# Kernel tuning notes

Hardware: AMD Instinct MI355X
Metric: run time of the kernel (lower is better)

The kernel has to match this reference:

```python
import math
import jax, jax.numpy as jnp
import numpy as np

B, Q, K = 1, 2048, 2048
CQ = CK = CV = 128
H, CH = 8, 32
HD = H * CH  # 256


def setup_inputs() -> dict:
    key = jax.random.key(0)
    ks = jax.random.split(key, 12)
    s = 0.02
    return {
        "q_x": jax.random.normal(ks[0], (B, Q, CQ), jnp.float32),
        "kv_x": jax.random.normal(ks[1], (B, K, CK), jnp.float32),
        "bias": jax.random.normal(ks[2], (B, 1, Q, K), jnp.float32),
        "distance": jax.random.uniform(ks[3], (B, Q, K, H), jnp.float32),
        "Wq": jax.random.normal(ks[4], (CQ, HD), jnp.float32) * s,
        "Wk": jax.random.normal(ks[5], (CK, HD), jnp.float32) * s,
        "Wv": jax.random.normal(ks[6], (CV, HD), jnp.float32) * s,
        "Wg": jax.random.normal(ks[7], (CQ, HD), jnp.float32) * s,
        "bg": jnp.zeros((HD,), jnp.float32),
        "Wo": jax.random.normal(ks[8], (HD, CQ), jnp.float32) * s,
        "bo": jnp.zeros((CQ,), jnp.float32),
    }


def reference(q_x, kv_x, bias, distance, Wq, Wk, Wv, Wg, bg, Wo, bo):
    # Projections -> [B, S, H, CH]
    q = (q_x @ Wq).reshape(B, Q, H, CH) / math.sqrt(CH)
    k = (kv_x @ Wk).reshape(B, K, H, CH)
    v = (kv_x @ Wv).reshape(B, K, H, CH)
    # Scores [B, H, Q, K]
    a = jnp.einsum("bqhc,bkhc->bhqk", q, k)
    a = a + bias
    # mha_permu=True: distance [B,Q,K,H] -> [B,H,Q,K]; rel_dis_pair_bias='add'
    a = a + jnp.transpose(distance, (0, 3, 1, 2))
    a = jax.nn.softmax(a, axis=-1)
    o = jnp.einsum("bhqk,bkhc->bqhc", a, v)  # [B, Q, H, CH]
    # Gating
    g = jax.nn.sigmoid(q_x @ Wg + bg).reshape(B, Q, H, CH)
    o = o * g
    o = o.reshape(B, Q, HD)
    return o @ Wo + bo
```

## Files before the change

kernel.cpp:

```cpp
#include <hip/hip_runtime.h>
#include <hip/hip_bf16.h>

#define Qn 2048
#define Kn 2048
#define Cin 128
#define Hn 8
#define CHn 32
#define HDn 256
#define NSPLIT 8
#define KP 68

typedef __attribute__((ext_vector_type(8))) short short8;
typedef __attribute__((ext_vector_type(4))) float f32x4;

static __device__ __forceinline__ unsigned short f2bf(float f) {
    unsigned int u = __float_as_uint(f);
    u += 0x7fffu + ((u >> 16) & 1u);
    return (unsigned short)(u >> 16);
}

__global__ __launch_bounds__(256) void proj_kernel(
    const float* __restrict__ qx, const float* __restrict__ kvx,
    const float* __restrict__ Wq, const float* __restrict__ Wk,
    const float* __restrict__ Wv, const float* __restrict__ Wg,
    const float* __restrict__ bg,
    unsigned short* __restrict__ qb, unsigned short* __restrict__ kb,
    unsigned short* __restrict__ vtb, float* __restrict__ gb)
{
    const int mat = blockIdx.y;
    const int r0 = blockIdx.x * 8;
    const int j = threadIdx.x;
    const float* A = (mat == 0 || mat == 3) ? qx : kvx;
    const float* W = (mat == 0) ? Wq : (mat == 1) ? Wk : (mat == 2) ? Wv : Wg;
    const float* Ar = A + r0 * Cin;
    float acc[8] = {0.f, 0.f, 0.f, 0.f, 0.f, 0.f, 0.f, 0.f};
    for (int c = 0; c < Cin; ++c) {
        const float w = W[c * HDn + j];
        #pragma unroll
        for (int i = 0; i < 8; ++i)
            acc[i] = fmaf(Ar[i * Cin + c], w, acc[i]);
    }
    if (mat == 0) {
        const float s = 0.17677669529663687f;
        #pragma unroll
        for (int i = 0; i < 8; ++i)
            qb[(r0 + i) * HDn + j] = f2bf(acc[i] * s);
    } else if (mat == 1) {
        #pragma unroll
        for (int i = 0; i < 8; ++i)
            kb[(r0 + i) * HDn + j] = f2bf(acc[i]);
    } else if (mat == 2) {
        unsigned short tmp[8];
        #pragma unroll
        for (int i = 0; i < 8; ++i) tmp[i] = f2bf(acc[i]);
        *(short8*)(vtb + (size_t)j * Kn + r0) = *(short8*)tmp;
    } else {
        const float b = bg[j];
        #pragma unroll
        for (int i = 0; i < 8; ++i)
            gb[(r0 + i) * HDn + j] = 1.f / (1.f + __expf(-(acc[i] + b)));
    }
}

__global__ __launch_bounds__(512, 5) void attn_kernel(
    const unsigned short* __restrict__ qb, const unsigned short* __restrict__ kb,
    const unsigned short* __restrict__ vtb,
    const float* __restrict__ bias, const float* __restrict__ dist,
    float* __restrict__ opart, float* __restrict__ lpart)
{
    __shared__ unsigned short ps[Hn][16][72];
    __shared__ _Float16 dbl[Hn * 16 * KP];

    const int bx = blockIdx.x;
    const int qt = bx >> 3;
    const int sp = bx & 7;
    const int q0 = qt * 16;
    const int k00 = sp * 256;
    const int t = threadIdx.x;
    const int h = t >> 6;
    const int l = t & 63;
    const int g = l >> 4;
    const int n = l & 15;

    const int sk = (t >> 1) & 63;
    const int shg = t & 1;
    const int sqb = t >> 7;

    const short8 qf = *(const short8*)(qb + (q0 + n) * HDn + h * CHn + g * 8);

    f32x4 o0 = {0.f, 0.f, 0.f, 0.f};
    f32x4 o1 = {0.f, 0.f, 0.f, 0.f};
    float lacc[4] = {0.f, 0.f, 0.f, 0.f};
    unsigned short* psh = &ps[h][0][0];
    const f32x4 z = {0.f, 0.f, 0.f, 0.f};

    f32x4 dv[4];
    float bv[4];
    #pragma unroll
    for (int i = 0; i < 4; ++i) {
        const int qi = q0 + sqb + 4 * i;
        dv[i] = *(const f32x4*)(dist + ((size_t)qi * Kn + k00 + sk) * Hn + 4 * shg);
        bv[i] = bias[(size_t)qi * Kn + k00 + sk];
    }

    for (int kt = 0; kt < 4; ++kt) {
        const int k0 = k00 + kt * 64;
        asm volatile("s_waitcnt lgkmcnt(0)\n\ts_barrier" ::: "memory");
        #pragma unroll
        for (int i = 0; i < 4; ++i) {
            const int qi = sqb + 4 * i;
            #pragma unroll
            for (int j = 0; j < 4; ++j)
                dbl[((shg * 4 + j) * 16 + qi) * KP + sk] = (_Float16)(dv[i][j] + bv[i]);
        }
        asm volatile("s_waitcnt lgkmcnt(0)\n\ts_barrier" ::: "memory");

        short8 kf[4];
        #pragma unroll
        for (int kkg = 0; kkg < 4; ++kkg)
            kf[kkg] = *(const short8*)(kb + (k0 + kkg * 16 + n) * HDn + h * CHn + g * 8);
        short8 vf[4];
        #pragma unroll
        for (int chunk = 0; chunk < 2; ++chunk) {
            vf[chunk * 2]     = *(const short8*)(vtb + (h * CHn + n) * Kn + k0 + chunk * 32 + g * 8);
            vf[chunk * 2 + 1] = *(const short8*)(vtb + (h * CHn + 16 + n) * Kn + k0 + chunk * 32 + g * 8);
        }
        __builtin_amdgcn_sched_barrier(0);
        if (kt < 3) {
            #pragma unroll
            for (int i = 0; i < 4; ++i) {
                const int qi = q0 + sqb + 4 * i;
                dv[i] = *(const f32x4*)(dist + ((size_t)qi * Kn + k0 + 64 + sk) * Hn + 4 * shg);
                bv[i] = bias[(size_t)qi * Kn + k0 + 64 + sk];
            }
        }

        f32x4 sf[4];
        #pragma unroll
        for (int kkg = 0; kkg < 4; ++kkg)
            sf[kkg] = __builtin_amdgcn_mfma_f32_16x16x32_bf16(qf, kf[kkg], z, 0, 0, 0);
        const _Float16* dbh = dbl + h * 16 * KP;
        #pragma unroll
        for (int kkg = 0; kkg < 4; ++kkg) {
            #pragma unroll
            for (int r = 0; r < 4; ++r) {
                const float db = (float)dbh[(g * 4 + r) * KP + kkg * 16 + n];
                const float p = __expf(sf[kkg][r] + db);
                sf[kkg][r] = p;
                lacc[r] += p;
            }
        }
        #pragma unroll
        for (int kkg = 0; kkg < 4; ++kkg) {
            #pragma unroll
            for (int r = 0; r < 4; ++r)
                psh[(g * 4 + r) * 72 + kkg * 16 + n] = f2bf(sf[kkg][r]);
        }
        #pragma unroll
        for (int chunk = 0; chunk < 2; ++chunk) {
            const short8 pf = *(const short8*)(psh + n * 72 + chunk * 32 + g * 8);
            o0 = __builtin_amdgcn_mfma_f32_16x16x32_bf16(pf, vf[chunk * 2], o0, 0, 0, 0);
            o1 = __builtin_amdgcn_mfma_f32_16x16x32_bf16(pf, vf[chunk * 2 + 1], o1, 0, 0, 0);
        }
    }
    float* op = opart + (size_t)sp * (Qn * HDn);
    #pragma unroll
    for (int r = 0; r < 4; ++r) {
        const int qg = q0 + g * 4 + r;
        op[qg * HDn + h * CHn + n] = o0[r];
        op[qg * HDn + h * CHn + 16 + n] = o1[r];
        float v = lacc[r];
        v += __shfl_xor(v, 1);
        v += __shfl_xor(v, 2);
        v += __shfl_xor(v, 4);
        v += __shfl_xor(v, 8);
        lacc[r] = v;
    }
    if (n == 0) {
        float* lp = lpart + (size_t)sp * (Qn * Hn);
        #pragma unroll
        for (int r = 0; r < 4; ++r)
            lp[(q0 + g * 4 + r) * Hn + h] = lacc[r];
    }
}

__global__ __launch_bounds__(256) void mergeout_kernel(
    const float* __restrict__ opart, const float* __restrict__ lpart,
    const float* __restrict__ gb, const float* __restrict__ Wo,
    const float* __restrict__ bo, float* __restrict__ out)
{
    __shared__ float olds[HDn];
    __shared__ float red[4][128];
    const int q = blockIdx.x;
    const int t = threadIdx.x;
    const int h = t >> 5;
    float s = 0.f;
    #pragma unroll
    for (int sp = 0; sp < NSPLIT; ++sp)
        s += opart[(size_t)sp * (Qn * HDn) + q * HDn + t];
    float lt = 0.f;
    #pragma unroll
    for (int sp = 0; sp < NSPLIT; ++sp)
        lt += lpart[(size_t)sp * (Qn * Hn) + q * Hn + h];
    olds[t] = (s / lt) * gb[q * HDn + t];
    __syncthreads();
    const int p = t & 63;
    const int seg = t >> 6;
    float a0 = 0.f, a1 = 0.f;
    for (int c = seg * 64; c < seg * 64 + 64; ++c) {
        const float ov = olds[c];
        const float2 w = *(const float2*)(Wo + c * Cin + 2 * p);
        a0 = fmaf(ov, w.x, a0);
        a1 = fmaf(ov, w.y, a1);
    }
    red[seg][2 * p] = a0;
    red[seg][2 * p + 1] = a1;
    __syncthreads();
    if (t < 128)
        out[q * Cin + t] = red[0][t] + red[1][t] + red[2][t] + red[3][t] + bo[t];
}

extern "C" void kernel_launch(void* const* d_in, const int* in_sizes, int n_in,
                              void* d_out, int out_size, void* d_ws, size_t ws_size,
                              hipStream_t stream)
{
    const float* qx   = (const float*)d_in[0];
    const float* kvx  = (const float*)d_in[1];
    const float* bias = (const float*)d_in[2];
    const float* dist = (const float*)d_in[3];
    const float* Wq   = (const float*)d_in[4];
    const float* Wk   = (const float*)d_in[5];
    const float* Wv   = (const float*)d_in[6];
    const float* Wg   = (const float*)d_in[7];
    const float* bg   = (const float*)d_in[8];
    const float* Wo   = (const float*)d_in[9];
    const float* bo   = (const float*)d_in[10];
    float* out = (float*)d_out;

    char* w = (char*)d_ws;
    unsigned short* qb  = (unsigned short*)(w);
    unsigned short* kb  = (unsigned short*)(w + (1ull << 20));
    unsigned short* vtb = (unsigned short*)(w + (2ull << 20));
    float* gb    = (float*)(w + (3ull << 20));
    float* opart = (float*)(w + (5ull << 20));
    float* lpart = (float*)(w + (21ull << 20));

    proj_kernel<<<dim3(Qn / 8, 4), 256, 0, stream>>>(qx, kvx, Wq, Wk, Wv, Wg, bg, qb, kb, vtb, gb);
    attn_kernel<<<dim3(128 * NSPLIT), 512, 0, stream>>>(qb, kb, vtb, bias, dist, opart, lpart);
    mergeout_kernel<<<dim3(Qn), 256, 0, stream>>>(opart, lpart, gb, Wo, bo, out);
}
```

Before: 273.6 us.

## Load distance and bias directly per lane, dropping LDS staging and barriers

Removes the shared-memory staging buffer for distance+bias and the two block barriers per K tile. Each lane now loads its own distance and bias scalars straight from global memory in the MFMA output layout. It also fully unrolls the K-tile loop and lowers the occupancy hint from 5 to 4 blocks per SM. The cost is uncoalesced scalar loads: distance is read with a stride of 8 floats, so memory efficiency drops. Prefetching of the next tile is also lost, which risks exposing load latency.

```diff
diff --git a/kernel.cpp b/kernel.cpp
--- a/kernel.cpp
+++ b/kernel.cpp
@@ -8,7 +8,6 @@
 #define CHn 32
 #define HDn 256
 #define NSPLIT 8
-#define KP 68
 
 typedef __attribute__((ext_vector_type(8))) short short8;
 typedef __attribute__((ext_vector_type(4))) float f32x4;
@@ -62,14 +61,13 @@
     }
 }
 
-__global__ __launch_bounds__(512, 5) void attn_kernel(
+__global__ __launch_bounds__(512, 4) void attn_kernel(
     const unsigned short* __restrict__ qb, const unsigned short* __restrict__ kb,
     const unsigned short* __restrict__ vtb,
     const float* __restrict__ bias, const float* __restrict__ dist,
     float* __restrict__ opart, float* __restrict__ lpart)
 {
     __shared__ unsigned short ps[Hn][16][72];
-    __shared__ _Float16 dbl[Hn * 16 * KP];
 
     const int bx = blockIdx.x;
     const int qt = bx >> 3;
@@ -82,10 +80,6 @@
     const int g = l >> 4;
     const int n = l & 15;
 
-    const int sk = (t >> 1) & 63;
-    const int shg = t & 1;
-    const int sqb = t >> 7;
-
     const short8 qf = *(const short8*)(qb + (q0 + n) * HDn + h * CHn + g * 8);
 
     f32x4 o0 = {0.f, 0.f, 0.f, 0.f};
@@ -94,26 +88,12 @@
     unsigned short* psh = &ps[h][0][0];
     const f32x4 z = {0.f, 0.f, 0.f, 0.f};
 
-    f32x4 dv[4];
-    float bv[4];
-    #pragma unroll
-    for (int i = 0; i < 4; ++i) {
-        const int qi = q0 + sqb + 4 * i;
-        dv[i] = *(const f32x4*)(dist + ((size_t)qi * Kn + k00 + sk) * Hn + 4 * shg);
-        bv[i] = bias[(size_t)qi * Kn + k00 + sk];
-    }
-
+    const float* dbase = dist + ((size_t)(q0 + g * 4) * Kn + k00 + n) * Hn + h;
+    const float* bbase = bias + (size_t)(q0 + g * 4) * Kn + k00 + n;
+
+    #pragma unroll
     for (int kt = 0; kt < 4; ++kt) {
         const int k0 = k00 + kt * 64;
-        asm volatile("s_waitcnt lgkmcnt(0)\n\ts_barrier" ::: "memory");
-        #pragma unroll
-        for (int i = 0; i < 4; ++i) {
-            const int qi = sqb + 4 * i;
-            #pragma unroll
-            for (int j = 0; j < 4; ++j)
-                dbl[((shg * 4 + j) * 16 + qi) * KP + sk] = (_Float16)(dv[i][j] + bv[i]);
-        }
-        asm volatile("s_waitcnt lgkmcnt(0)\n\ts_barrier" ::: "memory");
 
         short8 kf[4];
         #pragma unroll
@@ -126,12 +106,14 @@
             vf[chunk * 2 + 1] = *(const short8*)(vtb + (h * CHn + 16 + n) * Kn + k0 + chunk * 32 + g * 8);
         }
         __builtin_amdgcn_sched_barrier(0);
-        if (kt < 3) {
+
+        float db[16], bb[16];
+        #pragma unroll
+        for (int r = 0; r < 4; ++r) {
             #pragma unroll
-            for (int i = 0; i < 4; ++i) {
-                const int qi = q0 + sqb + 4 * i;
-                dv[i] = *(const f32x4*)(dist + ((size_t)qi * Kn + k0 + 64 + sk) * Hn + 4 * shg);
-                bv[i] = bias[(size_t)qi * Kn + k0 + 64 + sk];
+            for (int kk = 0; kk < 4; ++kk) {
+                db[r * 4 + kk] = dbase[((size_t)r * Kn + kt * 64 + kk * 16) * Hn];
+                bb[r * 4 + kk] = bbase[(size_t)r * Kn + kt * 64 + kk * 16];
             }
         }
 
@@ -139,23 +121,24 @@
         #pragma unroll
         for (int kkg = 0; kkg < 4; ++kkg)
             sf[kkg] = __builtin_amdgcn_mfma_f32_16x16x32_bf16(qf, kf[kkg], z, 0, 0, 0);
-        const _Float16* dbh = dbl + h * 16 * KP;
+
         #pragma unroll
         for (int kkg = 0; kkg < 4; ++kkg) {
             #pragma unroll
             for (int r = 0; r < 4; ++r) {
-                const float db = (float)dbh[(g * 4 + r) * KP + kkg * 16 + n];
-                const float p = __expf(sf[kkg][r] + db);
+                const float p = __expf(sf[kkg][r] + db[r * 4 + kkg] + bb[r * 4 + kkg]);
                 sf[kkg][r] = p;
                 lacc[r] += p;
             }
         }
+
         #pragma unroll
         for (int kkg = 0; kkg < 4; ++kkg) {
             #pragma unroll
             for (int r = 0; r < 4; ++r)
                 psh[(g * 4 + r) * 72 + kkg * 16 + n] = f2bf(sf[kkg][r]);
         }
+
         #pragma unroll
         for (int chunk = 0; chunk < 2; ++chunk) {
             const short8 pf = *(const short8*)(psh + n * 72 + chunk * 32 + g * 8);
@@ -163,6 +146,7 @@
             o1 = __builtin_amdgcn_mfma_f32_16x16x32_bf16(pf, vf[chunk * 2 + 1], o1, 0, 0, 0);
         }
     }
+
     float* op = opart + (size_t)sp * (Qn * HDn);
     #pragma unroll
     for (int r = 0; r < 4; ++r) {
```

New measurement: 318.6 us. 1.16x slower.
